# Kernel tuning notes

Measured on AMD Instinct MI355X. Metric: run time of the kernel, lower is better.

The kernel has to match this reference:

```python
import jax, jax.numpy as jnp
import numpy as np


def setup_inputs() -> dict:
    key = jax.random.key(0)
    k1, k2, k3, k4 = jax.random.split(key, 4)
    B, T, C, H = 32, 2048, 384, 64
    x = jax.random.normal(k1, (B, T, C), dtype=jnp.float32)
    # nn.Linear(C, H, bias=False): weight stored [H, C], applied as x @ W.T.
    # We store the transposed [C, H] form directly.
    s = 1.0 / np.sqrt(C)
    Wk = jax.random.normal(k2, (C, H), dtype=jnp.float32) * s
    Wq = jax.random.normal(k3, (C, H), dtype=jnp.float32) * s
    Wv = jax.random.normal(k4, (C, H), dtype=jnp.float32) * s
    return {"x": x, "Wk": Wk, "Wq": Wq, "Wv": Wv}


def reference(x, Wk, Wq, Wv):
    # x: [B, T, C]; Wk/Wq/Wv: [C, H]
    T = x.shape[1]
    H = Wk.shape[1]
    k = jnp.einsum('btc,ch->bth', x, Wk)
    q = jnp.einsum('btc,ch->bth', x, Wq)
    v = jnp.einsum('btc,ch->bth', x, Wv)
    scale = H ** (-0.5)
    scores = jnp.einsum('bth,bsh->bts', q, k) * scale  # [B, T, T]
    causal = jnp.tril(jnp.ones((T, T), dtype=bool))
    scores = jnp.where(causal, scores, -jnp.inf)
    attn = jax.nn.softmax(scores, axis=-1)
    # dropout is identity in eval mode
    out = jnp.einsum('bts,bsh->bth', attn, v)  # [B, T, H]
    return out
```

## Files before the change

### kernel.cpp

```cpp
#include <hip/hip_runtime.h>

typedef __bf16 bf16_8 __attribute__((ext_vector_type(8)));
typedef __bf16 bf16_4 __attribute__((ext_vector_type(4)));
typedef float  f32x4  __attribute__((ext_vector_type(4)));

#define NB 32
#define NT 2048
#define NC 384
#define NH 64

static __device__ __forceinline__ f32x4 mfma16(bf16_8 a, bf16_8 b, f32x4 c) {
  return __builtin_amdgcn_mfma_f32_16x16x32_bf16(a, b, c, 0, 0, 0);
}

__global__ void pack_w_kernel(const float* __restrict__ Wk, const float* __restrict__ Wq,
                              const float* __restrict__ Wv, __bf16* __restrict__ Wt) {
  int idx = blockIdx.x * 256 + threadIdx.x;
  if (idx >= 192 * NC) return;
  int n = idx / NC, k = idx % NC;
  int sel = n >> 6, h = n & 63;
  const float* W = (sel == 0) ? Wq : (sel == 1 ? Wk : Wv);
  float v = W[k * NH + h];
  if (sel == 0) v *= 0.125f * 1.44269504088896f;
  Wt[idx] = (__bf16)v;
}

__launch_bounds__(1024, 4)
__global__ void qkv_kernel(const float* __restrict__ x, const __bf16* __restrict__ Wt,
                           __bf16* __restrict__ Q, __bf16* __restrict__ K,
                           __bf16* __restrict__ Vt) {
  __shared__ __bf16 Wl[192 * 384];

  const int tid  = threadIdx.x;
  const int lane = tid & 63, wq = tid >> 6;
  const int quad = lane >> 4, l16 = lane & 15;
  const int rowblk = blockIdx.x * 256;
  const int rbase  = rowblk + wq * 16;
  const int row    = rbase + l16;

  #pragma unroll
  for (int i = 0; i < 9; ++i) {
    int g = tid + i * 1024;
    int r = g / 48, c = g - r * 48;
    int p = c ^ (r & 7);
    uint4 v = ((const uint4*)Wt)[g];
    *(uint4*)&Wl[(r * 48 + p) * 8] = v;
  }
  __syncthreads();

  f32x4 acc[12];
  #pragma unroll
  for (int n = 0; n < 12; ++n) acc[n] = f32x4{0.f, 0.f, 0.f, 0.f};

  const float* xrow = x + (size_t)row * NC;
  f32x4 xp0[4], xp1[4];
  #pragma unroll
  for (int d = 0; d < 4; ++d) {
    xp0[d] = *(const f32x4*)(xrow + d * 32 + quad * 8);
    xp1[d] = *(const f32x4*)(xrow + d * 32 + quad * 8 + 4);
  }

  #pragma unroll
  for (int kc = 0; kc < 12; ++kc) {
    const int slot = kc & 3;
    bf16_8 a;
    a[0] = (__bf16)xp0[slot][0]; a[1] = (__bf16)xp0[slot][1];
    a[2] = (__bf16)xp0[slot][2]; a[3] = (__bf16)xp0[slot][3];
    a[4] = (__bf16)xp1[slot][0]; a[5] = (__bf16)xp1[slot][1];
    a[6] = (__bf16)xp1[slot][2]; a[7] = (__bf16)xp1[slot][3];
    if (kc + 4 < 12) {
      const float* xp = xrow + (kc + 4) * 32 + quad * 8;
      xp0[slot] = *(const f32x4*)xp;
      xp1[slot] = *(const f32x4*)(xp + 4);
    }
    const int pc = (kc * 4 + quad) ^ (l16 & 7);
    const int cbase = l16 * 48 + pc;
    #pragma unroll
    for (int n = 0; n < 12; ++n) {
      bf16_8 b = *(const bf16_8*)&Wl[(n * 16 * 48 + cbase) * 8];
      acc[n] = mfma16(a, b, acc[n]);
    }
  }

  #pragma unroll
  for (int n = 0; n < 8; ++n)
    #pragma unroll
    for (int r = 0; r < 4; ++r) {
      int orow = rbase + quad * 4 + r;
      int h = (n & 3) * 16 + l16;
      __bf16 bv = (__bf16)acc[n][r];
      if (n < 4) Q[(size_t)orow * NH + h] = bv;
      else       K[(size_t)orow * NH + h] = bv;
    }

  __syncthreads();
  __bf16 (*Vl)[264] = (__bf16(*)[264])Wl;
  #pragma unroll
  for (int n = 8; n < 12; ++n) {
    int h = (n - 8) * 16 + l16;
    int t0 = wq * 16 + quad * 4;
    bf16_4 p;
    p[0] = (__bf16)acc[n][0]; p[1] = (__bf16)acc[n][1];
    p[2] = (__bf16)acc[n][2]; p[3] = (__bf16)acc[n][3];
    *(bf16_4*)&Vl[h][t0] = p;
  }
  __syncthreads();
  {
    int h = tid >> 4, seg = tid & 15;
    int bb = rowblk >> 11, t0 = (rowblk & (NT - 1)) + seg * 16;
    const __bf16* src = &Vl[h][seg * 16];
    __bf16* dst = Vt + ((size_t)(bb * NH + h)) * NT + t0;
    ((uint4*)dst)[0] = ((const uint4*)src)[0];
    ((uint4*)dst)[1] = ((const uint4*)src)[1];
  }
}

__launch_bounds__(256, 2)
__global__ void attn_kernel(const __bf16* __restrict__ Q, const __bf16* __restrict__ K,
                            const __bf16* __restrict__ Vt, float* __restrict__ out) {
  __shared__ __bf16 Ks[128][72];
  __shared__ __bf16 Vs[64][136];
  __shared__ __bf16 Ps[4][16][136];

  const int tid  = threadIdx.x;
  const int lane = tid & 63, wq = tid >> 6;
  const int quad = lane >> 4, l16 = lane & 15;
  const int b    = blockIdx.x >> 4;
  const int pair = blockIdx.x & 15;

  const float NEG_INF = -__builtin_inff();
  const int kr = tid >> 1, kc4 = (tid & 1) * 32;
  const int vr = tid >> 2, vc  = (tid & 3) * 32;
  const __bf16* Kg = K  + (size_t)b * NT * NH;
  const __bf16* Vg = Vt + (size_t)b * NH * NT;

  for (int pass = 0; pass < 2; ++pass) {
    const int qt = pass ? pair : (31 - pair);
    const int q0 = qt * 64;
    const int nSuper = (qt + 2) >> 1;

    const __bf16* qrow = Q + ((size_t)(b * NT + q0 + wq * 16 + l16)) * NH + quad * 8;
    bf16_8 qf0 = *(const bf16_8*)qrow;
    bf16_8 qf1 = *(const bf16_8*)(qrow + 32);

    f32x4 o[4];
    #pragma unroll
    for (int i = 0; i < 4; ++i) o[i] = f32x4{0.f, 0.f, 0.f, 0.f};
    float m_i = NEG_INF, l_i = 0.f;

    {
      const uint4* kp = (const uint4*)(Kg + (size_t)kr * NH + kc4);
      const uint4* vp = (const uint4*)(Vg + (size_t)vr * NT + vc);
      uint4 pk0 = kp[0], pk1 = kp[1], pk2 = kp[2], pk3 = kp[3];
      uint4 pv0 = vp[0], pv1 = vp[1], pv2 = vp[2], pv3 = vp[3];
      *(uint4*)&Ks[kr][kc4]      = pk0; *(uint4*)&Ks[kr][kc4 + 8]  = pk1;
      *(uint4*)&Ks[kr][kc4 + 16] = pk2; *(uint4*)&Ks[kr][kc4 + 24] = pk3;
      *(uint4*)&Vs[vr][vc]       = pv0; *(uint4*)&Vs[vr][vc + 8]   = pv1;
      *(uint4*)&Vs[vr][vc + 16]  = pv2; *(uint4*)&Vs[vr][vc + 24]  = pv3;
    }

    for (int i = 0; i < nSuper; ++i) {
      const bool more = (i + 1 < nSuper);
      uint4 pk[4], pv[4];
      if (more) {
        const int s0n = (i + 1) * 128;
        const uint4* kp = (const uint4*)(Kg + (size_t)(s0n + kr) * NH + kc4);
        pk[0] = kp[0]; pk[1] = kp[1]; pk[2] = kp[2]; pk[3] = kp[3];
        const uint4* vp = (const uint4*)(Vg + (size_t)vr * NT + s0n + vc);
        pv[0] = vp[0]; pv[1] = vp[1]; pv[2] = vp[2]; pv[3] = vp[3];
      }
      __syncthreads();

      f32x4 sv[8];
      #pragma unroll
      for (int st = 0; st < 8; ++st) {
        bf16_8 a0 = *(const bf16_8*)&Ks[st * 16 + l16][quad * 8];
        bf16_8 a1 = *(const bf16_8*)&Ks[st * 16 + l16][quad * 8 + 32];
        f32x4 accv = f32x4{0.f, 0.f, 0.f, 0.f};
        accv = mfma16(a0, qf0, accv);
        accv = mfma16(a1, qf1, accv);
        sv[st] = accv;
      }

      if (i == nSuper - 1) {
        int slimit = q0 + wq * 16 + l16 - i * 128;
        #pragma unroll
        for (int st = 0; st < 8; ++st)
          #pragma unroll
          for (int rr = 0; rr < 4; ++rr) {
            int sloc = st * 16 + quad * 4 + rr;
            if (sloc > slimit) sv[st][rr] = NEG_INF;
          }
      }

      float mx = NEG_INF;
      #pragma unroll
      for (int st = 0; st < 8; ++st)
        #pragma unroll
        for (int rr = 0; rr < 4; ++rr) mx = fmaxf(mx, sv[st][rr]);
      mx = fmaxf(mx, __shfl_xor(mx, 16));
      mx = fmaxf(mx, __shfl_xor(mx, 32));
      float m_new = fmaxf(m_i, mx);
      float alpha = __builtin_amdgcn_exp2f(m_i - m_new);

      float lsum = 0.f;
      #pragma unroll
      for (int st = 0; st < 8; ++st) {
        bf16_4 pkv;
        #pragma unroll
        for (int rr = 0; rr < 4; ++rr) {
          float p = __builtin_amdgcn_exp2f(sv[st][rr] - m_new);
          lsum += p;
          pkv[rr] = (__bf16)p;
        }
        *(bf16_4*)&Ps[wq][l16][st * 16 + quad * 4] = pkv;
      }
      lsum += __shfl_xor(lsum, 16);
      lsum += __shfl_xor(lsum, 32);
      l_i = l_i * alpha + lsum;
      m_i = m_new;

      f32x4 av;
      #pragma unroll
      for (int rr = 0; rr < 4; ++rr) av[rr] = __shfl(alpha, quad * 4 + rr);
      #pragma unroll
      for (int nt = 0; nt < 4; ++nt)
        #pragma unroll
        for (int rr = 0; rr < 4; ++rr) o[nt][rr] *= av[rr];

      bf16_8 pa[4];
      #pragma unroll
      for (int c = 0; c < 4; ++c)
        pa[c] = *(const bf16_8*)&Ps[wq][l16][c * 32 + quad * 8];
      #pragma unroll
      for (int nt = 0; nt < 4; ++nt) {
        #pragma unroll
        for (int c = 0; c < 4; ++c) {
          bf16_8 bv = *(const bf16_8*)&Vs[nt * 16 + l16][c * 32 + quad * 8];
          o[nt] = mfma16(pa[c], bv, o[nt]);
        }
      }

      __syncthreads();
      if (more) {
        *(uint4*)&Ks[kr][kc4]      = pk[0]; *(uint4*)&Ks[kr][kc4 + 8]  = pk[1];
        *(uint4*)&Ks[kr][kc4 + 16] = pk[2]; *(uint4*)&Ks[kr][kc4 + 24] = pk[3];
        *(uint4*)&Vs[vr][vc]       = pv[0]; *(uint4*)&Vs[vr][vc + 8]   = pv[1];
        *(uint4*)&Vs[vr][vc + 16]  = pv[2]; *(uint4*)&Vs[vr][vc + 24]  = pv[3];
      }
    }

    f32x4 lv;
    #pragma unroll
    for (int rr = 0; rr < 4; ++rr) lv[rr] = 1.f / __shfl(l_i, quad * 4 + rr);
    float* op = out + ((size_t)(b * NT + q0 + wq * 16 + quad * 4)) * NH + l16;
    #pragma unroll
    for (int nt = 0; nt < 4; ++nt)
      #pragma unroll
      for (int rr = 0; rr < 4; ++rr)
        op[(size_t)rr * NH + nt * 16] = o[nt][rr] * lv[rr];
  }
}

extern "C" void kernel_launch(void* const* d_in, const int* in_sizes, int n_in,
                              void* d_out, int out_size, void* d_ws, size_t ws_size,
                              hipStream_t stream) {
  const float* x  = (const float*)d_in[0];
  const float* Wk = (const float*)d_in[1];
  const float* Wq = (const float*)d_in[2];
  const float* Wv = (const float*)d_in[3];
  float* out = (float*)d_out;

  char* ws = (char*)d_ws;
  __bf16* Wt  = (__bf16*)ws;
  __bf16* Qb  = (__bf16*)(ws + 256 * 1024);
  __bf16* Kb  = Qb + (size_t)NB * NT * NH;
  __bf16* Vtb = Kb + (size_t)NB * NT * NH;

  pack_w_kernel<<<288, 256, 0, stream>>>(Wk, Wq, Wv, Wt);
  qkv_kernel<<<256, 1024, 0, stream>>>(x, Wt, Qb, Kb, Vtb);
  attn_kernel<<<NB * 16, 256, 0, stream>>>(Qb, Kb, Vtb, out);
}
```

Measured before the change: 257.7 us.

## Use 128-row query tiles with 8 waves and skip masked diagonal MFMAs

The attention kernel now uses 512-thread blocks with 8 waves covering a 128-row query tile instead of 64, so each 128-key K/V tile loaded to LDS serves twice as many queries. The block count is halved and the paired-tile load balancing is rescaled to 16 tiles per batch. On the diagonal tile, each wave skips QK and PV MFMAs for key sub-blocks that are fully masked. The cost is fewer blocks (256) on a large GPU, which may underfill the CUs, plus higher per-block LDS use.

```diff
diff --git a/kernel.cpp b/kernel.cpp
--- a/kernel.cpp
+++ b/kernel.cpp
@@ -115,29 +115,29 @@
   }
 }
 
-__launch_bounds__(256, 2)
+__launch_bounds__(512, 2)
 __global__ void attn_kernel(const __bf16* __restrict__ Q, const __bf16* __restrict__ K,
                             const __bf16* __restrict__ Vt, float* __restrict__ out) {
   __shared__ __bf16 Ks[128][72];
   __shared__ __bf16 Vs[64][136];
-  __shared__ __bf16 Ps[4][16][136];
+  __shared__ __bf16 Ps[8][16][136];
 
   const int tid  = threadIdx.x;
   const int lane = tid & 63, wq = tid >> 6;
   const int quad = lane >> 4, l16 = lane & 15;
-  const int b    = blockIdx.x >> 4;
-  const int pair = blockIdx.x & 15;
+  const int b    = blockIdx.x >> 3;
+  const int pair = blockIdx.x & 7;
 
   const float NEG_INF = -__builtin_inff();
-  const int kr = tid >> 1, kc4 = (tid & 1) * 32;
-  const int vr = tid >> 2, vc  = (tid & 3) * 32;
+  const int kr = tid >> 2, kc = (tid & 3) * 16;
+  const int vr = tid >> 3, vc = (tid & 7) * 16;
   const __bf16* Kg = K  + (size_t)b * NT * NH;
   const __bf16* Vg = Vt + (size_t)b * NH * NT;
 
   for (int pass = 0; pass < 2; ++pass) {
-    const int qt = pass ? pair : (31 - pair);
-    const int q0 = qt * 64;
-    const int nSuper = (qt + 2) >> 1;
+    const int jpos = pass ? pair : (15 - pair);
+    const int q0 = jpos * 128;
+    const int nSuper = jpos + 1;
 
     const __bf16* qrow = Q + ((size_t)(b * NT + q0 + wq * 16 + l16)) * NH + quad * 8;
     bf16_8 qf0 = *(const bf16_8*)qrow;
@@ -149,48 +149,53 @@
     float m_i = NEG_INF, l_i = 0.f;
 
     {
-      const uint4* kp = (const uint4*)(Kg + (size_t)kr * NH + kc4);
+      const uint4* kp = (const uint4*)(Kg + (size_t)kr * NH + kc);
+      uint4 k0 = kp[0], k1 = kp[1];
       const uint4* vp = (const uint4*)(Vg + (size_t)vr * NT + vc);
-      uint4 pk0 = kp[0], pk1 = kp[1], pk2 = kp[2], pk3 = kp[3];
-      uint4 pv0 = vp[0], pv1 = vp[1], pv2 = vp[2], pv3 = vp[3];
-      *(uint4*)&Ks[kr][kc4]      = pk0; *(uint4*)&Ks[kr][kc4 + 8]  = pk1;
-      *(uint4*)&Ks[kr][kc4 + 16] = pk2; *(uint4*)&Ks[kr][kc4 + 24] = pk3;
-      *(uint4*)&Vs[vr][vc]       = pv0; *(uint4*)&Vs[vr][vc + 8]   = pv1;
-      *(uint4*)&Vs[vr][vc + 16]  = pv2; *(uint4*)&Vs[vr][vc + 24]  = pv3;
+      uint4 v0 = vp[0], v1 = vp[1];
+      *(uint4*)&Ks[kr][kc]     = k0; *(uint4*)&Ks[kr][kc + 8] = k1;
+      *(uint4*)&Vs[vr][vc]     = v0; *(uint4*)&Vs[vr][vc + 8] = v1;
     }
 
     for (int i = 0; i < nSuper; ++i) {
       const bool more = (i + 1 < nSuper);
-      uint4 pk[4], pv[4];
+      const bool diag = (i == nSuper - 1);
+      uint4 pk[2], pv[2];
       if (more) {
         const int s0n = (i + 1) * 128;
-        const uint4* kp = (const uint4*)(Kg + (size_t)(s0n + kr) * NH + kc4);
-        pk[0] = kp[0]; pk[1] = kp[1]; pk[2] = kp[2]; pk[3] = kp[3];
+        const uint4* kp = (const uint4*)(Kg + (size_t)(s0n + kr) * NH + kc);
+        pk[0] = kp[0]; pk[1] = kp[1];
         const uint4* vp = (const uint4*)(Vg + (size_t)vr * NT + s0n + vc);
-        pv[0] = vp[0]; pv[1] = vp[1]; pv[2] = vp[2]; pv[3] = vp[3];
+        pv[0] = vp[0]; pv[1] = vp[1];
       }
       __syncthreads();
 
+      const int stMax = diag ? (wq + 1) : 8;
       f32x4 sv[8];
       #pragma unroll
       for (int st = 0; st < 8; ++st) {
-        bf16_8 a0 = *(const bf16_8*)&Ks[st * 16 + l16][quad * 8];
-        bf16_8 a1 = *(const bf16_8*)&Ks[st * 16 + l16][quad * 8 + 32];
-        f32x4 accv = f32x4{0.f, 0.f, 0.f, 0.f};
-        accv = mfma16(a0, qf0, accv);
-        accv = mfma16(a1, qf1, accv);
-        sv[st] = accv;
-      }
-
-      if (i == nSuper - 1) {
-        int slimit = q0 + wq * 16 + l16 - i * 128;
+        if (st < stMax) {
+          bf16_8 a0 = *(const bf16_8*)&Ks[st * 16 + l16][quad * 8];
+          bf16_8 a1 = *(const bf16_8*)&Ks[st * 16 + l16][quad * 8 + 32];
+          f32x4 accv = f32x4{0.f, 0.f, 0.f, 0.f};
+          accv = mfma16(a0, qf0, accv);
+          accv = mfma16(a1, qf1, accv);
+          sv[st] = accv;
+        } else {
+          sv[st] = f32x4{NEG_INF, NEG_INF, NEG_INF, NEG_INF};
+        }
+      }
+
+      if (diag) {
+        int slimit = wq * 16 + l16;
         #pragma unroll
         for (int st = 0; st < 8; ++st)
-          #pragma unroll
-          for (int rr = 0; rr < 4; ++rr) {
-            int sloc = st * 16 + quad * 4 + rr;
-            if (sloc > slimit) sv[st][rr] = NEG_INF;
-          }
+          if (st < stMax)
+            #pragma unroll
+            for (int rr = 0; rr < 4; ++rr) {
+              int sloc = st * 16 + quad * 4 + rr;
+              if (sloc > slimit) sv[st][rr] = NEG_INF;
+            }
       }
 
       float mx = NEG_INF;
@@ -228,25 +233,23 @@
         #pragma unroll
         for (int rr = 0; rr < 4; ++rr) o[nt][rr] *= av[rr];
 
-      bf16_8 pa[4];
-      #pragma unroll
-      for (int c = 0; c < 4; ++c)
-        pa[c] = *(const bf16_8*)&Ps[wq][l16][c * 32 + quad * 8];
-      #pragma unroll
-      for (int nt = 0; nt < 4; ++nt) {
-        #pragma unroll
-        for (int c = 0; c < 4; ++c) {
-          bf16_8 bv = *(const bf16_8*)&Vs[nt * 16 + l16][c * 32 + quad * 8];
-          o[nt] = mfma16(pa[c], bv, o[nt]);
+      const int cMax = diag ? ((wq >> 1) + 1) : 4;
+      #pragma unroll
+      for (int c = 0; c < 4; ++c) {
+        if (c < cMax) {
+          bf16_8 pa = *(const bf16_8*)&Ps[wq][l16][c * 32 + quad * 8];
+          #pragma unroll
+          for (int nt = 0; nt < 4; ++nt) {
+            bf16_8 bv = *(const bf16_8*)&Vs[nt * 16 + l16][c * 32 + quad * 8];
+            o[nt] = mfma16(pa, bv, o[nt]);
+          }
         }
       }
 
       __syncthreads();
       if (more) {
-        *(uint4*)&Ks[kr][kc4]      = pk[0]; *(uint4*)&Ks[kr][kc4 + 8]  = pk[1];
-        *(uint4*)&Ks[kr][kc4 + 16] = pk[2]; *(uint4*)&Ks[kr][kc4 + 24] = pk[3];
-        *(uint4*)&Vs[vr][vc]       = pv[0]; *(uint4*)&Vs[vr][vc + 8]   = pv[1];
-        *(uint4*)&Vs[vr][vc + 16]  = pv[2]; *(uint4*)&Vs[vr][vc + 24]  = pv[3];
+        *(uint4*)&Ks[kr][kc]     = pk[0]; *(uint4*)&Ks[kr][kc + 8] = pk[1];
+        *(uint4*)&Vs[vr][vc]     = pv[0]; *(uint4*)&Vs[vr][vc + 8] = pv[1];
       }
     }
 
@@ -279,5 +282,5 @@
 
   pack_w_kernel<<<288, 256, 0, stream>>>(Wk, Wq, Wv, Wt);
   qkv_kernel<<<256, 1024, 0, stream>>>(x, Wt, Qb, Kb, Vtb);
-  attn_kernel<<<NB * 16, 256, 0, stream>>>(Qb, Kb, Vtb, out);
-}
+  attn_kernel<<<NB * 8, 512, 0, stream>>>(Qb, Kb, Vtb, out);
+}
```

Result: faster. 239.6 us (-7.0%).
